# Optimization experiments

Measured on AMD Instinct MI355X. Metric: run time of the kernel, lower is better.

Reference implementation:

```python
import jax, jax.numpy as jnp
import numpy as np

NEG = -1000000.0  # mask fill value used by the original sequence_mask


def setup_inputs() -> dict:
    key = jax.random.key(0)
    k1, k2, k3, k4 = jax.random.split(key, 4)
    B, Nq, Nk, D = 8, 2048, 2048, 64
    queries = jax.random.normal(k1, (B, Nq, D), dtype=jnp.float32)
    keys = jax.random.normal(k2, (B, Nk, D), dtype=jnp.float32)
    values = jax.random.normal(k3, (B, Nk, D), dtype=jnp.float32)
    valid_lens = jax.random.randint(k4, (B,), 1, Nk + 1, dtype=jnp.int32)
    return {"queries": queries, "keys": keys, "values": values, "valid_lens": valid_lens}


def reference(queries, keys, values, valid_lens):
    d = queries.shape[-1]
    # scores: (B, n_q, n_k)
    scores = jnp.einsum("bqd,bkd->bqk", queries, keys) / jnp.sqrt(jnp.float32(d))
    # mask key positions >= valid_len (per-batch valid length, broadcast over queries)
    nk = scores.shape[-1]
    key_pos = jnp.arange(nk, dtype=jnp.int32)  # (n_k,)
    mask = key_pos[None, None, :] < valid_lens[:, None, None]  # (B, 1->n_q, n_k)
    scores = jnp.where(mask, scores, NEG)
    attn = jax.nn.softmax(scores, axis=-1)
    # dropout is identity in inference mode (no training flag in the original call)
    return jnp.einsum("bqk,bkd->bqd", attn, values)
```

## Files before the change

### kernel.cpp

```cpp
#include <hip/hip_runtime.h>
#include <hip/hip_bf16.h>


typedef __attribute__((ext_vector_type(8))) short bf16x8;
typedef __attribute__((ext_vector_type(8))) unsigned short u16x8;
typedef __attribute__((ext_vector_type(4))) float f32x4;

#define NQ 2048
#define NK 2048
#define DH 64
#define NB 8
#define NSPLIT 16
#define SPLIT_LEN 128
#define L2E 1.44269504088896341f
#define PSTRIDE 36

#define VMCNT(n) asm volatile("s_waitcnt vmcnt(" #n ")" ::: "memory")

__device__ __forceinline__ unsigned short f2bf(float f) {
    union { float f; unsigned int u; } v; v.f = f;
    unsigned int u = v.u;
    u += 0x7FFFu + ((u >> 16) & 1u);
    return (unsigned short)(u >> 16);
}
__device__ __forceinline__ float bf2f(unsigned short u) {
    union { unsigned int u; float f; } v; v.u = ((unsigned int)u) << 16; return v.f;
}
__device__ __forceinline__ unsigned int pack_bf2(float lo, float hi) {
    return ((unsigned int)f2bf(hi) << 16) | (unsigned int)f2bf(lo);
}
__device__ __forceinline__ float fast_exp2(float x) {
#if __has_builtin(__builtin_amdgcn_exp2f)
    return __builtin_amdgcn_exp2f(x);
#else
    return exp2f(x);
#endif
}
__device__ __forceinline__ void gload16(const void* g, void* l) {
    __builtin_amdgcn_global_load_lds(
        (const __attribute__((address_space(1))) void*)g,
        (__attribute__((address_space(3))) void*)l, 16, 0, 0);
}

__global__ __launch_bounds__(256) void prep(const float* __restrict__ K,
                                            const float* __restrict__ Q,
                                            const float* __restrict__ V,
                                            unsigned short* __restrict__ Kbf,
                                            unsigned short* __restrict__ Qbf,
                                            unsigned short* __restrict__ Vt) {
    if (blockIdx.x < 1024) {
        const bool isQ = blockIdx.x >= 512;
        const size_t idx = ((size_t)(blockIdx.x & 511) * 256 + threadIdx.x) * 8;
        const float* src = isQ ? Q : K;
        const float sc = isQ ? 0.125f : 1.0f;
        const float4 a = *reinterpret_cast<const float4*>(src + idx);
        const float4 b = *reinterpret_cast<const float4*>(src + idx + 4);
        bf16x8 o;
        o[0] = (short)f2bf(a.x * sc); o[1] = (short)f2bf(a.y * sc);
        o[2] = (short)f2bf(a.z * sc); o[3] = (short)f2bf(a.w * sc);
        o[4] = (short)f2bf(b.x * sc); o[5] = (short)f2bf(b.y * sc);
        o[6] = (short)f2bf(b.z * sc); o[7] = (short)f2bf(b.w * sc);
        *reinterpret_cast<bf16x8*>((isQ ? Qbf : Kbf) + idx) = o;
    } else {
        __shared__ unsigned short T[64][65];
        const int bid2 = blockIdx.x - 1024;
        const int b  = bid2 >> 5;
        const int k0 = (bid2 & 31) * 64;
        const int t  = threadIdx.x;
        const int r  = t >> 2;
        const int cb = (t & 3) * 16;
        const float* src = V + ((size_t)(b * NK + k0 + r)) * DH + cb;
#pragma unroll
        for (int j4 = 0; j4 < 4; ++j4) {
            const float4 v = *reinterpret_cast<const float4*>(src + j4 * 4);
            T[r][cb + j4 * 4 + 0] = f2bf(v.x);
            T[r][cb + j4 * 4 + 1] = f2bf(v.y);
            T[r][cb + j4 * 4 + 2] = f2bf(v.z);
            T[r][cb + j4 * 4 + 3] = f2bf(v.w);
        }
        __syncthreads();
        unsigned short* dstb = Vt + (size_t)b * DH * NK;
#pragma unroll
        for (int i = 0; i < 2; ++i) {
            const int cc = t + i * 256;
            const int d  = cc >> 3;
            const int kb = (cc & 7) * 8;
            bf16x8 o;
#pragma unroll
            for (int j = 0; j < 8; ++j) o[j] = (short)T[kb + j][d];
            *reinterpret_cast<bf16x8*>(dstb + (size_t)d * NK + k0 + kb) = o;
        }
    }
}

__global__ __launch_bounds__(512, 8) void attn_split(
    const unsigned short* __restrict__ Qbf, const unsigned short* __restrict__ Kbf,
    const unsigned short* __restrict__ Vt, const int* __restrict__ VL,
    float* __restrict__ Lsum, unsigned short* __restrict__ Opart)
{
    __shared__ __align__(16) unsigned char MEM[32768 + 2304];

    const int bid = blockIdx.x;
    const int x   = bid & 7;
    const int k   = bid >> 3;
    const int qg  = k & 15;
    const int cs  = k >> 4;
    const int b   = cs & 7;
    const int s   = ((x - b) & 7) + (cs >> 3) * 8;

    const int vlen  = VL[b];
    const int kv_lo = s * SPLIT_LEN;
    if (kv_lo >= vlen) return;
    const int kv_hi = min(vlen, kv_lo + SPLIT_LEN);
    const int chunk = kv_hi - kv_lo;

    const int tid  = threadIdx.x;
    const int wv   = tid >> 6;
    const int lane = tid & 63;
    const int g = lane >> 4;
    const int c = lane & 15;
    const int qt = qg * 8 + wv;
    const int swl = (c & 7) << 4;

    const unsigned short* Qb = Qbf + ((size_t)b * NQ + qt * 16) * DH;
    const unsigned char* Kc = (const unsigned char*)(Kbf + ((size_t)b * NK + kv_lo) * DH);
    const unsigned char* Vbase = (const unsigned char*)(Vt + (size_t)b * DH * NK);
    const int vk0b = kv_lo * 2;
    unsigned int* Pw = (unsigned int*)(wv < 7 ? MEM + wv * (PSTRIDE * 16 * 4)
                                              : MEM + 32768);

    bf16x8 qf[2];
#pragma unroll
    for (int ks = 0; ks < 2; ++ks)
        qf[ks] = *reinterpret_cast<const bf16x8*>(Qb + (size_t)c * DH + ks * 32 + g * 8);
#pragma unroll
    for (int i = 0; i < 2; ++i) {
        const int p = i * 8192 + tid * 16;
        const int a = p ^ (((p >> 7) & 7) << 4);
        gload16(Kc + a, MEM + p);
    }
#pragma unroll
    for (int i = 0; i < 2; ++i) {
        const int p = i * 8192 + tid * 16;
        const int a = p ^ (((p >> 8) & 7) << 4);
        const int d  = a >> 8;
        const int ko = a & 255;
        gload16(Vbase + (size_t)d * (NK * 2) + vk0b + ko, MEM + 16384 + p);
    }

    const int ntt = (chunk + 63) >> 6;

    VMCNT(2);
    __builtin_amdgcn_s_barrier();
    __builtin_amdgcn_sched_barrier(0);

    float l_run = 0.f;

    auto qk_tile = [&](int tt, unsigned int* pk) {
        f32x4 sv[4];
#pragma unroll
        for (int nt4 = 0; nt4 < 4; ++nt4) {
            const int aK = (tt * 64 + nt4 * 16 + c) * 128 + g * 16;
            const bf16x8 kf0 = *reinterpret_cast<const bf16x8*>(MEM + (aK ^ swl));
            const bf16x8 kf1 = *reinterpret_cast<const bf16x8*>(MEM + ((aK + 64) ^ swl));
            f32x4 tacc = (f32x4){0.f, 0.f, 0.f, 0.f};
            tacc = __builtin_amdgcn_mfma_f32_16x16x32_bf16(kf0, qf[0], tacc, 0, 0, 0);
            tacc = __builtin_amdgcn_mfma_f32_16x16x32_bf16(kf1, qf[1], tacc, 0, 0, 0);
            sv[nt4] = tacc;
        }
        const int kv0 = kv_lo + (tt << 6);
        if (kv0 + 64 > kv_hi) {
#pragma unroll
            for (int nt4 = 0; nt4 < 4; ++nt4)
#pragma unroll
                for (int r = 0; r < 4; ++r)
                    if (kv0 + nt4 * 16 + 4 * g + r >= vlen) sv[nt4][r] = -1e30f;
        }
        float rs = 0.f;
#pragma unroll
        for (int nt4 = 0; nt4 < 4; ++nt4)
#pragma unroll
            for (int r = 0; r < 4; ++r) {
                const float p = fast_exp2(sv[nt4][r] * L2E);
                sv[nt4][r] = p;
                rs += p;
            }
        l_run += rs;
#pragma unroll
        for (int nt4 = 0; nt4 < 4; ++nt4) {
            pk[nt4 * 2]     = pack_bf2(sv[nt4][0], sv[nt4][1]);
            pk[nt4 * 2 + 1] = pack_bf2(sv[nt4][2], sv[nt4][3]);
        }
    };

    unsigned int pkA[8], pkB[8];
    qk_tile(0, pkA);
    if (ntt > 1) qk_tile(1, pkB);

    VMCNT(0);
    __builtin_amdgcn_s_barrier();
    __builtin_amdgcn_sched_barrier(0);

    f32x4 acc[4];
#pragma unroll
    for (int i = 0; i < 4; ++i) acc[i] = (f32x4){0.f, 0.f, 0.f, 0.f};

    auto pv_tile = [&](int tt, const unsigned int* pk) {
#pragma unroll
        for (int nt4 = 0; nt4 < 4; ++nt4) {
            Pw[c * PSTRIDE + nt4 * 8 + 2 * g]     = pk[nt4 * 2];
            Pw[c * PSTRIDE + nt4 * 8 + 2 * g + 1] = pk[nt4 * 2 + 1];
        }
        asm volatile("s_waitcnt lgkmcnt(0)" ::: "memory");
        const bf16x8 pa0 = *reinterpret_cast<const bf16x8*>(&Pw[c * PSTRIDE + 4 * g]);
        const bf16x8 pa1 = *reinterpret_cast<const bf16x8*>(&Pw[c * PSTRIDE + 16 + 4 * g]);
#pragma unroll
        for (int ks2 = 0; ks2 < 2; ++ks2) {
            const bf16x8 pa = ks2 ? pa1 : pa0;
#pragma unroll
            for (int ntd = 0; ntd < 4; ++ntd) {
                const int aV = (ntd * 16 + c) * 256 + tt * 128 + ks2 * 64 + g * 16;
                const bf16x8 vf = *reinterpret_cast<const bf16x8*>(MEM + 16384 + (aV ^ swl));
                acc[ntd] = __builtin_amdgcn_mfma_f32_16x16x32_bf16(pa, vf, acc[ntd], 0, 0, 0);
            }
        }
        asm volatile("s_waitcnt lgkmcnt(0)" ::: "memory");
    };

    pv_tile(0, pkA);
    if (ntt > 1) pv_tile(1, pkB);

    float lf = l_run;
    lf += __shfl_xor(lf, 16);
    lf += __shfl_xor(lf, 32);

    const size_t pbase = (size_t)(b * NSPLIT + s) * 128 + qt;
    if (lane < 16) Lsum[pbase * 16 + c] = lf;

    u16x8 pk0, pk1;
#pragma unroll
    for (int ntd = 0; ntd < 2; ++ntd)
#pragma unroll
        for (int r = 0; r < 4; ++r) pk0[ntd * 4 + r] = f2bf(acc[ntd][r]);
#pragma unroll
    for (int ntd = 2; ntd < 4; ++ntd)
#pragma unroll
        for (int r = 0; r < 4; ++r) pk1[(ntd - 2) * 4 + r] = f2bf(acc[ntd][r]);
    unsigned short* op = Opart + pbase * 1024 + (size_t)lane * 16;
    *reinterpret_cast<u16x8*>(op)     = pk0;
    *reinterpret_cast<u16x8*>(op + 8) = pk1;
}

__global__ __launch_bounds__(256) void attn_merge(
    const float* __restrict__ Lsum, const unsigned short* __restrict__ Opart,
    const int* __restrict__ VL, float* __restrict__ O)
{
    const int tid  = threadIdx.x;
    const int wv   = tid >> 6;
    const int lane = tid & 63;
    const int g = lane >> 4;
    const int c = lane & 15;
    const int qi = blockIdx.x * 4 + wv;
    const int b  = qi >> 7;
    const int qt = qi & 127;
    const int vlen = VL[b];
    const int nact = min(NSPLIT, (vlen + SPLIT_LEN - 1) / SPLIT_LEN);

    float accv[16];
    float L4[4] = {0.f, 0.f, 0.f, 0.f};
#pragma unroll
    for (int j = 0; j < 16; ++j) accv[j] = 0.f;

    for (int s = 0; s < nact; ++s) {
        const size_t pb = (size_t)(b * NSPLIT + s) * 128 + qt;
        const u16x8* src = reinterpret_cast<const u16x8*>(
            Opart + pb * 1024 + (size_t)lane * 16);
        const u16x8 lo = src[0], hi = src[1];
#pragma unroll
        for (int j = 0; j < 8; ++j) {
            accv[j]     += bf2f(lo[j]);
            accv[8 + j] += bf2f(hi[j]);
        }
        const float* Lp = Lsum + pb * 16 + 4 * g;
#pragma unroll
        for (int r = 0; r < 4; ++r) L4[r] += Lp[r];
    }
    float inv4[4];
#pragma unroll
    for (int r = 0; r < 4; ++r) inv4[r] = 1.0f / L4[r];

    float* Ob = O + ((size_t)(b * NQ + qt * 16)) * DH;
#pragma unroll
    for (int ntd = 0; ntd < 4; ++ntd)
#pragma unroll
        for (int r = 0; r < 4; ++r)
            Ob[(size_t)(4 * g + r) * DH + ntd * 16 + c] = accv[ntd * 4 + r] * inv4[r];
}

__global__ __launch_bounds__(64) void attn_fwd(
    const float* __restrict__ Q, const float* __restrict__ K,
    const float* __restrict__ V, const int* __restrict__ VL,
    float* __restrict__ O)
{
    __shared__ __align__(16) unsigned short Plds[16 * 40];
    const int bid = blockIdx.x;
    const int b  = bid >> 7;
    const int qt = bid & 127;
    const int q0 = qt * 16;
    const int lane = threadIdx.x;
    const int g = lane >> 4;
    const int c = lane & 15;
    const float* Qb = Q + ((size_t)b * NQ + q0) * DH;
    const float* Kb = K + (size_t)b * NK * DH;
    const float* Vb = V + (size_t)b * NK * DH;
    const int vlen = VL[b];
    bf16x8 qf[2];
#pragma unroll
    for (int ks = 0; ks < 2; ++ks) {
        const float* src = Qb + (size_t)c * DH + ks * 32 + g * 8;
#pragma unroll
        for (int e = 0; e < 8; ++e) qf[ks][e] = (short)f2bf(src[e] * 0.125f);
    }
    f32x4 acc[4];
#pragma unroll
    for (int nt = 0; nt < 4; ++nt) acc[nt] = (f32x4){0.f,0.f,0.f,0.f};
    float m_run[4], l_run[4];
#pragma unroll
    for (int r = 0; r < 4; ++r) { m_run[r] = -3.0e38f; l_run[r] = 0.f; }
    const int ntiles = (vlen + 31) / 32;
    for (int kt = 0; kt < ntiles; ++kt) {
        const int kv0 = kt * 32;
        f32x4 s[2] = {{0.f,0.f,0.f,0.f},{0.f,0.f,0.f,0.f}};
#pragma unroll
        for (int nt = 0; nt < 2; ++nt) {
            const float* kp = Kb + (size_t)(kv0 + nt * 16 + c) * DH + g * 8;
#pragma unroll
            for (int ks = 0; ks < 2; ++ks) {
                bf16x8 kf;
#pragma unroll
                for (int e = 0; e < 8; ++e) kf[e] = (short)f2bf(kp[ks * 32 + e]);
                s[nt] = __builtin_amdgcn_mfma_f32_16x16x32_bf16(qf[ks], kf, s[nt], 0, 0, 0);
            }
        }
        const bool msk0 = (kv0 + c)      >= vlen;
        const bool msk1 = (kv0 + 16 + c) >= vlen;
#pragma unroll
        for (int r = 0; r < 4; ++r) {
            if (msk0) s[0][r] = -1e30f;
            if (msk1) s[1][r] = -1e30f;
        }
        float tmax[4];
#pragma unroll
        for (int r = 0; r < 4; ++r) tmax[r] = fmaxf(s[0][r], s[1][r]);
#pragma unroll
        for (int mbit = 1; mbit < 16; mbit <<= 1)
#pragma unroll
            for (int r = 0; r < 4; ++r)
                tmax[r] = fmaxf(tmax[r], __shfl_xor(tmax[r], mbit));
        float p0[4], p1[4];
#pragma unroll
        for (int r = 0; r < 4; ++r) {
            const float mn = fmaxf(m_run[r], tmax[r]);
            const float sc = fast_exp2((m_run[r] - mn) * L2E);
            m_run[r] = mn;
            p0[r] = fast_exp2((s[0][r] - mn) * L2E);
            p1[r] = fast_exp2((s[1][r] - mn) * L2E);
            l_run[r] = l_run[r] * sc + p0[r] + p1[r];
#pragma unroll
            for (int nt = 0; nt < 4; ++nt) acc[nt][r] *= sc;
        }
#pragma unroll
        for (int r = 0; r < 4; ++r) {
            Plds[(4 * g + r) * 40 + c]      = f2bf(p0[r]);
            Plds[(4 * g + r) * 40 + 16 + c] = f2bf(p1[r]);
        }
        asm volatile("s_waitcnt lgkmcnt(0)" ::: "memory");
        const bf16x8 pa = *reinterpret_cast<const bf16x8*>(&Plds[c * 40 + g * 8]);
#pragma unroll
        for (int nt = 0; nt < 4; ++nt) {
            bf16x8 vf;
#pragma unroll
            for (int e = 0; e < 8; ++e)
                vf[e] = (short)f2bf(Vb[(size_t)(kv0 + 8 * g + e) * DH + nt * 16 + c]);
            acc[nt] = __builtin_amdgcn_mfma_f32_16x16x32_bf16(pa, vf, acc[nt], 0, 0, 0);
        }
    }
#pragma unroll
    for (int mbit = 1; mbit < 16; mbit <<= 1)
#pragma unroll
        for (int r = 0; r < 4; ++r)
            l_run[r] += __shfl_xor(l_run[r], mbit);
    float* Ob = O + ((size_t)b * NQ + q0) * DH;
#pragma unroll
    for (int r = 0; r < 4; ++r) {
        const float inv = 1.0f / l_run[r];
#pragma unroll
        for (int nt = 0; nt < 4; ++nt)
            Ob[(size_t)(4 * g + r) * DH + nt * 16 + c] = acc[nt][r] * inv;
    }
}

extern "C" void kernel_launch(void* const* d_in, const int* in_sizes, int n_in,
                              void* d_out, int out_size, void* d_ws, size_t ws_size,
                              hipStream_t stream) {
    const float* Q  = (const float*)d_in[0];
    const float* K  = (const float*)d_in[1];
    const float* V  = (const float*)d_in[2];
    const int*   VL = (const int*)d_in[3];
    float* O = (float*)d_out;

    const size_t KB_OFF = 0;
    const size_t QB_OFF = (size_t)2 << 20;
    const size_t VT_OFF = (size_t)4 << 20;
    const size_t ML_OFF = (size_t)6 << 20;
    const size_t OP_OFF = (size_t)8 << 20;
    const size_t NEED   = OP_OFF + (size_t)NB * NSPLIT * 128 * 1024 * 2;

    if (ws_size >= NEED) {
        char* w = (char*)d_ws;
        unsigned short* Kbf   = (unsigned short*)(w + KB_OFF);
        unsigned short* Qbf   = (unsigned short*)(w + QB_OFF);
        unsigned short* Vtp   = (unsigned short*)(w + VT_OFF);
        float*          Lsum  = (float*)(w + ML_OFF);
        unsigned short* Opart = (unsigned short*)(w + OP_OFF);

        prep<<<1280, 256, 0, stream>>>(K, Q, V, Kbf, Qbf, Vtp);
        attn_split<<<NB * NSPLIT * 16, 512, 0, stream>>>(Qbf, Kbf, Vtp, VL, Lsum, Opart);
        attn_merge<<<256, 256, 0, stream>>>(Lsum, Opart, VL, O);
    } else {
        attn_fwd<<<NB * 128, 64, 0, stream>>>(Q, K, V, VL, O);
    }
}
```

Before: 32.12 us.

## Pipeline K/V loads per 64-key tile and repack P via ds_bpermute

Splits the K and V shared-memory staging into per-tile halves ordered K0,V0,K1,V1, so the first QK tile and first PV tile can start while later loads are still in flight, using staged vmcnt waits. It also replaces the per-wave LDS scratch round trip for the probability fragment with ds_bpermute register shuffles, removing the P scratch buffer and its waits. The cost is more barriers, a different V layout in LDS and extra bpermute instructions. The bpermute lane mapping has to reproduce the old transpose exactly.

```diff
diff --git a/kernel.cpp b/kernel.cpp
--- a/kernel.cpp
+++ b/kernel.cpp
@@ -13,7 +13,6 @@
 #define NSPLIT 16
 #define SPLIT_LEN 128
 #define L2E 1.44269504088896341f
-#define PSTRIDE 36
 
 #define VMCNT(n) asm volatile("s_waitcnt vmcnt(" #n ")" ::: "memory")
 
@@ -98,7 +97,7 @@
     const unsigned short* __restrict__ Vt, const int* __restrict__ VL,
     float* __restrict__ Lsum, unsigned short* __restrict__ Opart)
 {
-    __shared__ __align__(16) unsigned char MEM[32768 + 2304];
+    __shared__ __align__(16) unsigned char KV[32768];
 
     const int bid = blockIdx.x;
     const int x   = bid & 7;
@@ -113,6 +112,7 @@
     if (kv_lo >= vlen) return;
     const int kv_hi = min(vlen, kv_lo + SPLIT_LEN);
     const int chunk = kv_hi - kv_lo;
+    const int ntt   = (chunk + 63) >> 6;
 
     const int tid  = threadIdx.x;
     const int wv   = tid >> 6;
@@ -126,49 +126,40 @@
     const unsigned char* Kc = (const unsigned char*)(Kbf + ((size_t)b * NK + kv_lo) * DH);
     const unsigned char* Vbase = (const unsigned char*)(Vt + (size_t)b * DH * NK);
     const int vk0b = kv_lo * 2;
-    unsigned int* Pw = (unsigned int*)(wv < 7 ? MEM + wv * (PSTRIDE * 16 * 4)
-                                              : MEM + 32768);
+    const int a0 = ((2 * (g & 1)) * 16 + c) * 4;
+    const int a1 = a0 + 64;
 
     bf16x8 qf[2];
 #pragma unroll
     for (int ks = 0; ks < 2; ++ks)
         qf[ks] = *reinterpret_cast<const bf16x8*>(Qb + (size_t)c * DH + ks * 32 + g * 8);
-#pragma unroll
-    for (int i = 0; i < 2; ++i) {
-        const int p = i * 8192 + tid * 16;
+    __builtin_amdgcn_sched_barrier(0);
+    {
+        const int p = tid * 16;
         const int a = p ^ (((p >> 7) & 7) << 4);
-        gload16(Kc + a, MEM + p);
-    }
-#pragma unroll
-    for (int i = 0; i < 2; ++i) {
-        const int p = i * 8192 + tid * 16;
-        const int a = p ^ (((p >> 8) & 7) << 4);
-        const int d  = a >> 8;
-        const int ko = a & 255;
-        gload16(Vbase + (size_t)d * (NK * 2) + vk0b + ko, MEM + 16384 + p);
-    }
-
-    const int ntt = (chunk + 63) >> 6;
-
-    VMCNT(2);
-    __builtin_amdgcn_s_barrier();
-    __builtin_amdgcn_sched_barrier(0);
+        const int d = a >> 7, ko = a & 127;
+        gload16(Kc + a, KV + p);
+        gload16(Vbase + (size_t)d * (NK * 2) + vk0b + ko, KV + 8192 + p);
+        __builtin_amdgcn_sched_barrier(0);
+        gload16(Kc + 8192 + a, KV + 16384 + p);
+        gload16(Vbase + (size_t)d * (NK * 2) + vk0b + 128 + ko, KV + 24576 + p);
+        __builtin_amdgcn_sched_barrier(0);
+    }
 
     float l_run = 0.f;
 
-    auto qk_tile = [&](int tt, unsigned int* pk) {
+    auto qk_tile = [&](const unsigned char* Kr, int kv0, unsigned int* pk) {
         f32x4 sv[4];
 #pragma unroll
         for (int nt4 = 0; nt4 < 4; ++nt4) {
-            const int aK = (tt * 64 + nt4 * 16 + c) * 128 + g * 16;
-            const bf16x8 kf0 = *reinterpret_cast<const bf16x8*>(MEM + (aK ^ swl));
-            const bf16x8 kf1 = *reinterpret_cast<const bf16x8*>(MEM + ((aK + 64) ^ swl));
+            const int aK = (nt4 * 16 + c) * 128 + g * 16;
+            const bf16x8 kf0 = *reinterpret_cast<const bf16x8*>(Kr + (aK ^ swl));
+            const bf16x8 kf1 = *reinterpret_cast<const bf16x8*>(Kr + ((aK + 64) ^ swl));
             f32x4 tacc = (f32x4){0.f, 0.f, 0.f, 0.f};
             tacc = __builtin_amdgcn_mfma_f32_16x16x32_bf16(kf0, qf[0], tacc, 0, 0, 0);
             tacc = __builtin_amdgcn_mfma_f32_16x16x32_bf16(kf1, qf[1], tacc, 0, 0, 0);
             sv[nt4] = tacc;
         }
-        const int kv0 = kv_lo + (tt << 6);
         if (kv0 + 64 > kv_hi) {
 #pragma unroll
             for (int nt4 = 0; nt4 < 4; ++nt4)
@@ -193,42 +184,62 @@
         }
     };
 
-    unsigned int pkA[8], pkB[8];
-    qk_tile(0, pkA);
-    if (ntt > 1) qk_tile(1, pkB);
+    auto repack = [&](const unsigned int* pk, bf16x8* pa) {
+#pragma unroll
+        for (int ks2 = 0; ks2 < 2; ++ks2) {
+            union { unsigned int u[4]; bf16x8 v; } out;
+#pragma unroll
+            for (int w = 0; w < 4; ++w) {
+                const int addr = (w >> 1) ? a1 : a0;
+                const int lo = __builtin_amdgcn_ds_bpermute(addr, (int)pk[4 * ks2 + (w & 1)]);
+                const int hi = __builtin_amdgcn_ds_bpermute(addr, (int)pk[4 * ks2 + 2 + (w & 1)]);
+                out.u[w] = (unsigned int)((g >> 1) ? hi : lo);
+            }
+            pa[ks2] = out.v;
+        }
+    };
+
+    f32x4 acc[4];
+#pragma unroll
+    for (int i = 0; i < 4; ++i) acc[i] = (f32x4){0.f, 0.f, 0.f, 0.f};
+
+    auto pv_tile = [&](const unsigned char* Vr, const bf16x8* pa) {
+#pragma unroll
+        for (int ks2 = 0; ks2 < 2; ++ks2)
+#pragma unroll
+            for (int ntd = 0; ntd < 4; ++ntd) {
+                const int aV = (ntd * 16 + c) * 128 + ks2 * 64 + g * 16;
+                const bf16x8 vf = *reinterpret_cast<const bf16x8*>(Vr + (aV ^ swl));
+                acc[ntd] = __builtin_amdgcn_mfma_f32_16x16x32_bf16(pa[ks2], vf, acc[ntd], 0, 0, 0);
+            }
+    };
+
+    VMCNT(3);
+    __builtin_amdgcn_s_barrier();
+    __builtin_amdgcn_sched_barrier(0);
+
+    unsigned int pkA[8];
+    bf16x8 paA[2];
+    qk_tile(KV, kv_lo, pkA);
+    repack(pkA, paA);
+
+    VMCNT(1);
+    __builtin_amdgcn_s_barrier();
+    __builtin_amdgcn_sched_barrier(0);
+
+    pv_tile(KV + 8192, paA);
+    bf16x8 paB[2];
+    if (ntt > 1) {
+        unsigned int pkB[8];
+        qk_tile(KV + 16384, kv_lo + 64, pkB);
+        repack(pkB, paB);
+    }
 
     VMCNT(0);
     __builtin_amdgcn_s_barrier();
     __builtin_amdgcn_sched_barrier(0);
 
-    f32x4 acc[4];
-#pragma unroll
-    for (int i = 0; i < 4; ++i) acc[i] = (f32x4){0.f, 0.f, 0.f, 0.f};
-
-    auto pv_tile = [&](int tt, const unsigned int* pk) {
-#pragma unroll
-        for (int nt4 = 0; nt4 < 4; ++nt4) {
-            Pw[c * PSTRIDE + nt4 * 8 + 2 * g]     = pk[nt4 * 2];
-            Pw[c * PSTRIDE + nt4 * 8 + 2 * g + 1] = pk[nt4 * 2 + 1];
-        }
-        asm volatile("s_waitcnt lgkmcnt(0)" ::: "memory");
-        const bf16x8 pa0 = *reinterpret_cast<const bf16x8*>(&Pw[c * PSTRIDE + 4 * g]);
-        const bf16x8 pa1 = *reinterpret_cast<const bf16x8*>(&Pw[c * PSTRIDE + 16 + 4 * g]);
-#pragma unroll
-        for (int ks2 = 0; ks2 < 2; ++ks2) {
-            const bf16x8 pa = ks2 ? pa1 : pa0;
-#pragma unroll
-            for (int ntd = 0; ntd < 4; ++ntd) {
-                const int aV = (ntd * 16 + c) * 256 + tt * 128 + ks2 * 64 + g * 16;
-                const bf16x8 vf = *reinterpret_cast<const bf16x8*>(MEM + 16384 + (aV ^ swl));
-                acc[ntd] = __builtin_amdgcn_mfma_f32_16x16x32_bf16(pa, vf, acc[ntd], 0, 0, 0);
-            }
-        }
-        asm volatile("s_waitcnt lgkmcnt(0)" ::: "memory");
-    };
-
-    pv_tile(0, pkA);
-    if (ntt > 1) pv_tile(1, pkB);
+    if (ntt > 1) pv_tile(KV + 24576, paB);
 
     float lf = l_run;
     lf += __shfl_xor(lf, 16);
```

Result: no change. 31.88 us, median of 2 (-0.7%).
